# Performance work log

Hardware: AMD Instinct MI355X
Metric: run time of the kernel (lower is better)

The kernel has to match this reference:

```python
import jax, jax.numpy as jnp
import numpy as np

B, H, S, D = 2, 16, 2048, 64

def setup_inputs() -> dict:
    key = jax.random.key(0)
    kq, kk, kv = jax.random.split(key, 3)
    q = jax.random.normal(kq, (B, H, S, D), dtype=jnp.float32)
    k = jax.random.normal(kk, (B, H, S, D), dtype=jnp.float32)
    v = jax.random.normal(kv, (B, H, S, D), dtype=jnp.float32)
    return {"q": q, "k": k, "v": v}

def reference(q, k, v):
    d_k = q.shape[-1]
    scale = 1.0 / jnp.sqrt(jnp.asarray(d_k, dtype=q.dtype))
    # scores: [B, H, Sq, Sk]
    scores = jnp.einsum("bhqd,bhkd->bhqk", q, k) * scale
    attn = jax.nn.softmax(scores, axis=-1)
    out = jnp.einsum("bhqk,bhkd->bhqd", attn, v)
    return out
```

## Files before the change

### kernel.cpp

```cpp
#include <hip/hip_runtime.h>
#include <math.h>

constexpr int Bc = 2, Hc = 16, Sc = 2048, Dc = 64;
constexpr int BQ = 128;
constexpr int BK = 64;
constexpr int NT = Sc / BK;

constexpr int KWD = 36;
constexpr int VWD = 33;
constexpr int KSD_OFF = 0;
constexpr int VTD_OFF = 2 * 64 * KWD;
constexpr int SMEM_DW = VTD_OFF + 2 * 64 * VWD;

typedef __attribute__((ext_vector_type(8))) short short8v;
typedef __attribute__((ext_vector_type(4))) float f32x4;
typedef __attribute__((ext_vector_type(4))) unsigned int uint4v;

__device__ __forceinline__ unsigned int cvt_pk_bf16(float lo, float hi) {
    unsigned int d;
    asm("v_cvt_pk_bf16_f32 %0, %1, %2" : "=v"(d) : "v"(lo), "v"(hi));
    return d;
}

__global__ __launch_bounds__(512, 4)
void attn_mfma_kernel(const float* __restrict__ Q,
                      const float* __restrict__ K,
                      const float* __restrict__ V,
                      float* __restrict__ O)
{
    __shared__ __align__(16) unsigned int smem[SMEM_DW];

    const int tid  = threadIdx.x;
    const int wave = tid >> 6;
    const int lane = tid & 63;
    const int n    = lane & 15;
    const int qd   = lane >> 4;
    const int qw   = wave & 3;
    const int kh   = wave >> 2;

    const int hid = blockIdx.x;
    const int hk  = hid >> 3;
    const int bh  = (hid & 7) + 8 * (hk >> 4);
    const int q0  = (hk & 15) * BQ;

    const float* Qg = Q + ((size_t)bh * Sc + q0) * Dc;
    const float* Kg = K + (size_t)bh * Sc * Dc;
    const float* Vg = V + (size_t)bh * Sc * Dc;
    float*       Og = O + ((size_t)bh * Sc + q0) * Dc;

    short8v q_frag[2][2];
#pragma unroll
    for (int qt = 0; qt < 2; ++qt)
#pragma unroll
        for (int kc = 0; kc < 2; ++kc) {
            const float* qrow = Qg + (qw * 32 + qt * 16 + n) * Dc + kc * 32 + qd * 8;
            float4 f0 = *reinterpret_cast<const float4*>(qrow);
            float4 f1 = *reinterpret_cast<const float4*>(qrow + 4);
            uint4v u;
            u[0] = cvt_pk_bf16(f0.x * 0.125f, f0.y * 0.125f);
            u[1] = cvt_pk_bf16(f0.z * 0.125f, f0.w * 0.125f);
            u[2] = cvt_pk_bf16(f1.x * 0.125f, f1.y * 0.125f);
            u[3] = cvt_pk_bf16(f1.z * 0.125f, f1.w * 0.125f);
            q_frag[qt][kc] = __builtin_bit_cast(short8v, u);
        }

    const f32x4 z = {0.f, 0.f, 0.f, 0.f};
    f32x4 o_acc[2][4] = {{z, z, z, z}, {z, z, z, z}};
    float l_part[2] = {0.f, 0.f};

    const int kr  = tid >> 3;
    const int kc8 = (tid & 7) << 3;
    const int vkp = tid >> 4;
    const int dpb = tid & 15;

    const float* kbase = Kg + kr * Dc + kc8;
    const float* vbase = Vg + vkp * 2 * Dc + dpb * 2;

    float4 ka[2];
    float2 va[2], vb[2];

    auto load_regs = [&](int kt) {
        const float* Kt = kbase + kt * (BK * Dc);
        const float* Vt = vbase + kt * (BK * Dc);
        ka[0] = *reinterpret_cast<const float4*>(Kt);
        ka[1] = *reinterpret_cast<const float4*>(Kt + 4);
#pragma unroll
        for (int i = 0; i < 2; ++i) {
            va[i] = *reinterpret_cast<const float2*>(Vt + 32 * i);
            vb[i] = *reinterpret_cast<const float2*>(Vt + Dc + 32 * i);
        }
    };
    auto write_lds = [&](int bb) {
        uint4v w;
        w[0] = cvt_pk_bf16(ka[0].x, ka[0].y);
        w[1] = cvt_pk_bf16(ka[0].z, ka[0].w);
        w[2] = cvt_pk_bf16(ka[1].x, ka[1].y);
        w[3] = cvt_pk_bf16(ka[1].z, ka[1].w);
        *reinterpret_cast<uint4v*>(
            &smem[KSD_OFF + bb * 64 * KWD + kr * KWD + (tid & 7) * 4]) = w;
        unsigned int* vd = &smem[VTD_OFF + bb * 64 * VWD];
#pragma unroll
        for (int i = 0; i < 2; ++i) {
            int dp = dpb + 16 * i;
            vd[(dp * 2)     * VWD + vkp] = cvt_pk_bf16(va[i].x, vb[i].x);
            vd[(dp * 2 + 1) * VWD + vkp] = cvt_pk_bf16(va[i].y, vb[i].y);
        }
    };

    auto compute = [&](int bb) {
        f32x4 st[2][2] = {{z, z}, {z, z}};
        const unsigned int* ks = &smem[KSD_OFF + bb * 64 * KWD];
        __builtin_amdgcn_s_setprio(1);
#pragma unroll
        for (int nt = 0; nt < 2; ++nt)
#pragma unroll
            for (int kc = 0; kc < 2; ++kc) {
                short8v kf = *reinterpret_cast<const short8v*>(
                    &ks[(kh * 32 + nt * 16 + n) * KWD + kc * 16 + qd * 4]);
#pragma unroll
                for (int qt = 0; qt < 2; ++qt)
                    st[qt][nt] = __builtin_amdgcn_mfma_f32_16x16x32_bf16(
                        kf, q_frag[qt][kc], st[qt][nt], 0, 0, 0);
            }
        __builtin_amdgcn_s_setprio(0);

        short8v p_frag[2];
#pragma unroll
        for (int qt = 0; qt < 2; ++qt) {
            float p00 = __expf(st[qt][0][0]), p01 = __expf(st[qt][0][1]);
            float p02 = __expf(st[qt][0][2]), p03 = __expf(st[qt][0][3]);
            float p10 = __expf(st[qt][1][0]), p11 = __expf(st[qt][1][1]);
            float p12 = __expf(st[qt][1][2]), p13 = __expf(st[qt][1][3]);
            l_part[qt] += ((p00 + p01) + (p02 + p03)) + ((p10 + p11) + (p12 + p13));

            unsigned int x0 = cvt_pk_bf16(p00, p01);
            unsigned int x1 = cvt_pk_bf16(p02, p03);
            unsigned int y0 = cvt_pk_bf16(p10, p11);
            unsigned int y1 = cvt_pk_bf16(p12, p13);
            asm("v_permlane32_swap_b32 %0, %1" : "+v"(x0), "+v"(y0));
            asm("v_permlane16_swap_b32 %0, %1" : "+v"(x0), "+v"(y0));
            asm("v_permlane32_swap_b32 %0, %1" : "+v"(x1), "+v"(y1));
            asm("v_permlane16_swap_b32 %0, %1" : "+v"(x1), "+v"(y1));
            uint4v pu; pu[0] = x0; pu[1] = x1; pu[2] = y0; pu[3] = y1;
            p_frag[qt] = __builtin_bit_cast(short8v, pu);
        }

        const unsigned int* vt = &smem[VTD_OFF + bb * 64 * VWD];
        __builtin_amdgcn_s_setprio(1);
#pragma unroll
        for (int dt = 0; dt < 4; ++dt) {
            const unsigned int* vrow = vt + (dt * 16 + n) * VWD + kh * 16 + qd * 4;
            uint4v vu;
            vu[0] = vrow[0]; vu[1] = vrow[1]; vu[2] = vrow[2]; vu[3] = vrow[3];
            short8v vf = __builtin_bit_cast(short8v, vu);
#pragma unroll
            for (int qt = 0; qt < 2; ++qt)
                o_acc[qt][dt] = __builtin_amdgcn_mfma_f32_16x16x32_bf16(
                    p_frag[qt], vf, o_acc[qt][dt], 0, 0, 0);
        }
        __builtin_amdgcn_s_setprio(0);
    };

    load_regs(0);
    write_lds(0);
    __syncthreads();

    int cur = 0;
    for (int kt = 0; kt < NT; ++kt) {
        const bool more = (kt + 1 < NT);
        if (more) load_regs(kt + 1);

        compute(cur);

        if (more) write_lds(cur ^ 1);
        __syncthreads();
        cur ^= 1;
    }

    float* mo = reinterpret_cast<float*>(smem);
    float* ml = reinterpret_cast<float*>(smem + 8192);
    if (kh == 1) {
#pragma unroll
        for (int qt = 0; qt < 2; ++qt) {
#pragma unroll
            for (int dt = 0; dt < 4; ++dt)
                *reinterpret_cast<f32x4*>(
                    &mo[(((qw * 64 + lane) * 2 + qt) * 4 + dt) * 4]) = o_acc[qt][dt];
            ml[(qw * 64 + lane) * 2 + qt] = l_part[qt];
        }
    }
    __syncthreads();
    if (kh == 0) {
#pragma unroll
        for (int qt = 0; qt < 2; ++qt) {
#pragma unroll
            for (int dt = 0; dt < 4; ++dt)
                o_acc[qt][dt] += *reinterpret_cast<const f32x4*>(
                    &mo[(((qw * 64 + lane) * 2 + qt) * 4 + dt) * 4]);
            l_part[qt] += ml[(qw * 64 + lane) * 2 + qt];
        }

#pragma unroll
        for (int qt = 0; qt < 2; ++qt) {
            float lp = l_part[qt];
            lp += __shfl_xor(lp, 16, 64);
            lp += __shfl_xor(lp, 32, 64);
#pragma unroll
            for (int r = 0; r < 4; ++r) {
                float lr  = __shfl(lp, qd * 4 + r, 64);
                float inv = 1.0f / lr;
#pragma unroll
                for (int dt = 0; dt < 4; ++dt) {
                    Og[(qw * 32 + qt * 16 + qd * 4 + r) * Dc + dt * 16 + n] =
                        o_acc[qt][dt][r] * inv;
                }
            }
        }
    }
}

extern "C" void kernel_launch(void* const* d_in, const int* in_sizes, int n_in,
                              void* d_out, int out_size, void* d_ws, size_t ws_size,
                              hipStream_t stream) {
    const float* q = (const float*)d_in[0];
    const float* k = (const float*)d_in[1];
    const float* v = (const float*)d_in[2];
    float*       o = (float*)d_out;

    dim3 grid((Sc / BQ) * Bc * Hc);
    attn_mfma_kernel<<<grid, 512, 0, stream>>>(q, k, v, o);
}
```

Measured before the change: 131.7 us.

## Precompute bf16 K/V tiles in workspace and stream via global_load_lds

Adds a prep kernel that converts K and V to bf16 once per call, with V transposed, into XOR-swizzled 8KB tiles in the workspace. The attention kernel then copies each tile straight into LDS with global_load_lds and no register staging, and reads it with swizzled addresses instead of padded strides. This removes the fp32 K/V traffic and the per-block conversion that was repeated for each of the 16 query blocks sharing a head. It costs an extra kernel launch and a workspace round trip.

```diff
diff --git a/kernel.cpp b/kernel.cpp
--- a/kernel.cpp
+++ b/kernel.cpp
@@ -6,11 +6,9 @@
 constexpr int BK = 64;
 constexpr int NT = Sc / BK;
 
-constexpr int KWD = 36;
-constexpr int VWD = 33;
-constexpr int KSD_OFF = 0;
-constexpr int VTD_OFF = 2 * 64 * KWD;
-constexpr int SMEM_DW = VTD_OFF + 2 * 64 * VWD;
+constexpr size_t WS_TILE  = 8192;
+constexpr size_t WS_BH    = (size_t)NT * WS_TILE;
+constexpr size_t WS_HALF  = (size_t)Bc * Hc * WS_BH;
 
 typedef __attribute__((ext_vector_type(8))) short short8v;
 typedef __attribute__((ext_vector_type(4))) float f32x4;
@@ -21,14 +19,65 @@
     asm("v_cvt_pk_bf16_f32 %0, %1, %2" : "=v"(d) : "v"(lo), "v"(hi));
     return d;
 }
+__device__ __forceinline__ unsigned short to_bf16(float f) {
+    unsigned int u = __float_as_uint(f);
+    return (unsigned short)((u + 0x7FFFu + ((u >> 16) & 1u)) >> 16);
+}
+__device__ __forceinline__ void gload16(const void* g, void* l) {
+    __builtin_amdgcn_global_load_lds(
+        (const __attribute__((address_space(1))) void*)g,
+        (__attribute__((address_space(3))) void*)l, 16, 0, 0);
+}
+
+__global__ __launch_bounds__(512, 2)
+void prep_kernel(const float* __restrict__ K, const float* __restrict__ V,
+                 unsigned char* __restrict__ ws)
+{
+    __shared__ unsigned short lv[4096];
+    const int tid = threadIdx.x;
+    const int b   = blockIdx.x;
+    const int r   = tid >> 3;
+    const int c8  = (tid & 7) * 8;
+
+    if (b < 1024) {
+        const int bh = b >> 5, t = b & 31;
+        const float* src = V + (((size_t)bh * Sc + t * BK) + r) * Dc + c8;
+        float4 f0 = *reinterpret_cast<const float4*>(src);
+        float4 f1 = *reinterpret_cast<const float4*>(src + 4);
+        float f[8] = {f0.x, f0.y, f0.z, f0.w, f1.x, f1.y, f1.z, f1.w};
+#pragma unroll
+        for (int m = 0; m < 8; ++m) {
+            int d = c8 + m;
+            lv[(d * 64 + r) ^ ((d & 7) << 3)] = to_bf16(f[m]);
+        }
+        __syncthreads();
+        uint4v w = *reinterpret_cast<const uint4v*>(&lv[tid * 8]);
+        *reinterpret_cast<uint4v*>(
+            ws + WS_HALF + ((size_t)bh * NT + t) * WS_TILE + tid * 16) = w;
+    } else {
+        const int b2 = b - 1024;
+        const int bh = b2 >> 5, t = b2 & 31;
+        const float* src = K + (((size_t)bh * Sc + t * BK) + r) * Dc + c8;
+        float4 f0 = *reinterpret_cast<const float4*>(src);
+        float4 f1 = *reinterpret_cast<const float4*>(src + 4);
+        uint4v w;
+        w[0] = cvt_pk_bf16(f0.x, f0.y);
+        w[1] = cvt_pk_bf16(f0.z, f0.w);
+        w[2] = cvt_pk_bf16(f1.x, f1.y);
+        w[3] = cvt_pk_bf16(f1.z, f1.w);
+        int byte = (r * 128 + (tid & 7) * 16) ^ ((r & 7) << 4);
+        *reinterpret_cast<uint4v*>(
+            ws + ((size_t)bh * NT + t) * WS_TILE + byte) = w;
+    }
+}
 
 __global__ __launch_bounds__(512, 4)
 void attn_mfma_kernel(const float* __restrict__ Q,
-                      const float* __restrict__ K,
-                      const float* __restrict__ V,
+                      const unsigned char* __restrict__ ws,
                       float* __restrict__ O)
 {
-    __shared__ __align__(16) unsigned int smem[SMEM_DW];
+    __shared__ __align__(16) unsigned int smem[8704];
+    unsigned char* sB = reinterpret_cast<unsigned char*>(smem);
 
     const int tid  = threadIdx.x;
     const int wave = tid >> 6;
@@ -44,9 +93,9 @@
     const int q0  = (hk & 15) * BQ;
 
     const float* Qg = Q + ((size_t)bh * Sc + q0) * Dc;
-    const float* Kg = K + (size_t)bh * Sc * Dc;
-    const float* Vg = V + (size_t)bh * Sc * Dc;
     float*       Og = O + ((size_t)bh * Sc + q0) * Dc;
+    const unsigned char* wsK = ws + (size_t)bh * WS_BH;
+    const unsigned char* wsV = ws + WS_HALF + (size_t)bh * WS_BH;
 
     short8v q_frag[2][2];
 #pragma unroll
@@ -68,55 +117,29 @@
     f32x4 o_acc[2][4] = {{z, z, z, z}, {z, z, z, z}};
     float l_part[2] = {0.f, 0.f};
 
-    const int kr  = tid >> 3;
-    const int kc8 = (tid & 7) << 3;
-    const int vkp = tid >> 4;
-    const int dpb = tid & 15;
-
-    const float* kbase = Kg + kr * Dc + kc8;
-    const float* vbase = Vg + vkp * 2 * Dc + dpb * 2;
-
-    float4 ka[2];
-    float2 va[2], vb[2];
-
-    auto load_regs = [&](int kt) {
-        const float* Kt = kbase + kt * (BK * Dc);
-        const float* Vt = vbase + kt * (BK * Dc);
-        ka[0] = *reinterpret_cast<const float4*>(Kt);
-        ka[1] = *reinterpret_cast<const float4*>(Kt + 4);
-#pragma unroll
-        for (int i = 0; i < 2; ++i) {
-            va[i] = *reinterpret_cast<const float2*>(Vt + 32 * i);
-            vb[i] = *reinterpret_cast<const float2*>(Vt + Dc + 32 * i);
-        }
-    };
-    auto write_lds = [&](int bb) {
-        uint4v w;
-        w[0] = cvt_pk_bf16(ka[0].x, ka[0].y);
-        w[1] = cvt_pk_bf16(ka[0].z, ka[0].w);
-        w[2] = cvt_pk_bf16(ka[1].x, ka[1].y);
-        w[3] = cvt_pk_bf16(ka[1].z, ka[1].w);
-        *reinterpret_cast<uint4v*>(
-            &smem[KSD_OFF + bb * 64 * KWD + kr * KWD + (tid & 7) * 4]) = w;
-        unsigned int* vd = &smem[VTD_OFF + bb * 64 * VWD];
-#pragma unroll
-        for (int i = 0; i < 2; ++i) {
-            int dp = dpb + 16 * i;
-            vd[(dp * 2)     * VWD + vkp] = cvt_pk_bf16(va[i].x, vb[i].x);
-            vd[(dp * 2 + 1) * VWD + vkp] = cvt_pk_bf16(va[i].y, vb[i].y);
-        }
-    };
-
-    auto compute = [&](int bb) {
+    gload16(wsK + tid * 16,         sB + tid * 16);
+    gload16(wsV + tid * 16,         sB + 16384 + tid * 16);
+    __syncthreads();
+
+    int buf = 0;
+    for (int kt = 0; kt < NT; ++kt) {
+        if (kt + 1 < NT) {
+            size_t src = (size_t)(kt + 1) * WS_TILE + tid * 16;
+            int dst = (buf ^ 1) * 8192 + tid * 16;
+            gload16(wsK + src, sB + dst);
+            gload16(wsV + src, sB + 16384 + dst);
+        }
+
+        const unsigned char* kb = sB + buf * 8192;
         f32x4 st[2][2] = {{z, z}, {z, z}};
-        const unsigned int* ks = &smem[KSD_OFF + bb * 64 * KWD];
         __builtin_amdgcn_s_setprio(1);
 #pragma unroll
         for (int nt = 0; nt < 2; ++nt)
 #pragma unroll
             for (int kc = 0; kc < 2; ++kc) {
-                short8v kf = *reinterpret_cast<const short8v*>(
-                    &ks[(kh * 32 + nt * 16 + n) * KWD + kc * 16 + qd * 4]);
+                int byte = ((kh * 32 + nt * 16 + n) * 128 + kc * 64 + qd * 16)
+                           ^ ((n & 7) << 4);
+                short8v kf = *reinterpret_cast<const short8v*>(kb + byte);
 #pragma unroll
                 for (int qt = 0; qt < 2; ++qt)
                     st[qt][nt] = __builtin_amdgcn_mfma_f32_16x16x32_bf16(
@@ -124,7 +147,7 @@
             }
         __builtin_amdgcn_s_setprio(0);
 
-        short8v p_frag[2];
+        short8v pf0, pf1;
 #pragma unroll
         for (int qt = 0; qt < 2; ++qt) {
             float p00 = __expf(st[qt][0][0]), p01 = __expf(st[qt][0][1]);
@@ -142,39 +165,25 @@
             asm("v_permlane32_swap_b32 %0, %1" : "+v"(x1), "+v"(y1));
             asm("v_permlane16_swap_b32 %0, %1" : "+v"(x1), "+v"(y1));
             uint4v pu; pu[0] = x0; pu[1] = x1; pu[2] = y0; pu[3] = y1;
-            p_frag[qt] = __builtin_bit_cast(short8v, pu);
-        }
-
-        const unsigned int* vt = &smem[VTD_OFF + bb * 64 * VWD];
+            if (qt == 0) pf0 = __builtin_bit_cast(short8v, pu);
+            else         pf1 = __builtin_bit_cast(short8v, pu);
+        }
+
+        const unsigned char* vb = sB + 16384 + buf * 8192;
         __builtin_amdgcn_s_setprio(1);
 #pragma unroll
         for (int dt = 0; dt < 4; ++dt) {
-            const unsigned int* vrow = vt + (dt * 16 + n) * VWD + kh * 16 + qd * 4;
-            uint4v vu;
-            vu[0] = vrow[0]; vu[1] = vrow[1]; vu[2] = vrow[2]; vu[3] = vrow[3];
-            short8v vf = __builtin_bit_cast(short8v, vu);
-#pragma unroll
-            for (int qt = 0; qt < 2; ++qt)
-                o_acc[qt][dt] = __builtin_amdgcn_mfma_f32_16x16x32_bf16(
-                    p_frag[qt], vf, o_acc[qt][dt], 0, 0, 0);
+            int byte = ((dt * 16 + n) * 128 + kh * 64 + qd * 16) ^ ((n & 7) << 4);
+            short8v vf = *reinterpret_cast<const short8v*>(vb + byte);
+            o_acc[0][dt] = __builtin_amdgcn_mfma_f32_16x16x32_bf16(
+                pf0, vf, o_acc[0][dt], 0, 0, 0);
+            o_acc[1][dt] = __builtin_amdgcn_mfma_f32_16x16x32_bf16(
+                pf1, vf, o_acc[1][dt], 0, 0, 0);
         }
         __builtin_amdgcn_s_setprio(0);
-    };
-
-    load_regs(0);
-    write_lds(0);
-    __syncthreads();
-
-    int cur = 0;
-    for (int kt = 0; kt < NT; ++kt) {
-        const bool more = (kt + 1 < NT);
-        if (more) load_regs(kt + 1);
-
-        compute(cur);
-
-        if (more) write_lds(cur ^ 1);
+
         __syncthreads();
-        cur ^= 1;
+        buf ^= 1;
     }
 
     float* mo = reinterpret_cast<float*>(smem);
@@ -226,7 +235,8 @@
     const float* k = (const float*)d_in[1];
     const float* v = (const float*)d_in[2];
     float*       o = (float*)d_out;
-
-    dim3 grid((Sc / BQ) * Bc * Hc);
-    attn_mfma_kernel<<<grid, 512, 0, stream>>>(q, k, v, o);
-}
+    unsigned char* ws = (unsigned char*)d_ws;
+
+    prep_kernel<<<dim3(2048), 512, 0, stream>>>(k, v, ws);
+    attn_mfma_kernel<<<dim3((Sc / BQ) * Bc * Hc), 512, 0, stream>>>(q, ws, o);
+}
```

Measured after the change: 133.6 us. No clear change (+1.4%).
